# Kernel optimization log

Measured on AMD Instinct MI355X. Metric: run time of the kernel, lower is better.

Reference implementation:

```python
import jax, jax.numpy as jnp
import numpy as np

EPSILON = 0.05
MAX_ITER = 50
ALPHA = 6.0
THRESHOLD = 0.25
SCALE = 0.02  # keeps OT costs near THRESHOLD so the gate is not saturated


def setup_inputs() -> dict:
    key = jax.random.key(0)
    k1, k2 = jax.random.split(key)
    B, E, D, P = 8192, 8, 512, 32
    tokens = jax.random.normal(k1, (B, E, D), dtype=jnp.float32) * SCALE
    prototypes = jax.random.normal(k2, (E, P, D), dtype=jnp.float32) * SCALE
    return {"tokens": tokens, "prototypes": prototypes, "full_index": 0}


def _sinkhorn_log(cost, epsilon, max_iter):
    # cost: [..., n_source, n_target]; batched log-domain Sinkhorn, fixed iterations
    ns, nt = cost.shape[-2], cost.shape[-1]
    log_mu = jnp.full(cost.shape[:-1], -float(np.log(ns)), dtype=cost.dtype)
    log_nu = jnp.full(cost.shape[:-2] + (nt,), -float(np.log(nt)), dtype=cost.dtype)
    log_k = -cost / epsilon

    def step(carry, _):
        log_u, log_v = carry
        log_u = log_mu - jax.scipy.special.logsumexp(log_k + log_v[..., None, :], axis=-1)
        log_v = log_nu - jax.scipy.special.logsumexp(log_k + log_u[..., :, None], axis=-2)
        return (log_u, log_v), None

    (log_u, log_v), _ = jax.lax.scan(
        step, (jnp.zeros_like(log_mu), jnp.zeros_like(log_nu)), None, length=max_iter
    )
    return jnp.exp(log_k + log_u[..., :, None] + log_v[..., None, :])


def reference(tokens, prototypes, full_index):
    # tokens: [B, E, D], prototypes: [E, P, D]
    B, E, D = tokens.shape
    anchor = tokens[:, full_index, :]                                   # [B, D]
    source = jnp.stack(
        [tokens, jnp.broadcast_to(anchor[:, None, :], tokens.shape)], axis=2
    )                                                                   # [B, E, 2, D]
    # squared euclidean cdist: ||s||^2 - 2 s.p + ||p||^2
    s2 = jnp.sum(source * source, axis=-1)                              # [B, E, 2]
    p2 = jnp.sum(prototypes * prototypes, axis=-1)                      # [E, P]
    cross = jnp.einsum('besd,epd->besp', source, prototypes)            # [B, E, 2, P]
    cost = jnp.maximum(s2[..., None] - 2.0 * cross + p2[None, :, None, :], 0.0)
    transport = _sinkhorn_log(cost, EPSILON, MAX_ITER)                  # [B, E, 2, P]
    ot_cost = jnp.sum(transport * cost, axis=(-1, -2))                  # [B, E]
    validity = jax.nn.sigmoid(-ALPHA * (ot_cost - THRESHOLD))[..., None]  # [B, E, 1]
    # the full_index expert always passes with validity 1 and zero cost
    is_full = jnp.arange(E) == full_index                               # [E]
    ot_cost = jnp.where(is_full[None, :], 0.0, ot_cost)
    validity = jnp.where(is_full[None, :, None], 1.0, validity)
    return validity, ot_cost
```

## Files before the change

### kernel.cpp

```cpp
#include <hip/hip_runtime.h>
#include <hip/hip_bf16.h>


#define EXP2F(x) __builtin_amdgcn_exp2f(x)
#define LOG2F(x) __builtin_amdgcn_logf(x)
#define RCPF(x)  __builtin_amdgcn_rcpf(x)

typedef __bf16 bf16x8 __attribute__((ext_vector_type(8)));
typedef float  f32x4  __attribute__((ext_vector_type(4)));

#define BDIM 8192
#define EDIM 8
#define DDIM 512
#define PDIM 32
#define BPB  32
#define NTHR 256
#define PFD  4
#define C_SCALE 28.853900817779268f
#define LOG2E   1.4426950408889634f

__device__ __forceinline__ bf16x8 cvt2(float4 a, float4 b) {
  bf16x8 r;
  r[0] = (__bf16)a.x; r[1] = (__bf16)a.y; r[2] = (__bf16)a.z; r[3] = (__bf16)a.w;
  r[4] = (__bf16)b.x; r[5] = (__bf16)b.y; r[6] = (__bf16)b.z; r[7] = (__bf16)b.w;
  return r;
}

__global__ __launch_bounds__(NTHR, 3)
void ot_noise_gate_kernel(const float* __restrict__ tokens,
                          const float* __restrict__ protos,
                          const int*   __restrict__ fullIndexPtr,
                          float*       __restrict__ out) {
  const int fi    = fullIndexPtr[0];
  const int e     = blockIdx.x & (EDIM - 1);
  const int b0    = (blockIdx.x >> 3) * BPB;
  float* outVal = out;
  float* outOt  = out + BDIM * EDIM;

  if (e == fi) {
    int t = threadIdx.x;
    if (t < BPB) {
      int b = b0 + t;
      outVal[b * EDIM + e] = 1.0f;
      outOt [b * EDIM + e] = 0.0f;
    }
    return;
  }

  __shared__ __align__(16) __bf16 sB[64 * PDIM * 8];
  __shared__ float sPNp[8][PDIM];
  __shared__ __align__(16) float sCw[4][16][36];

  const int t  = threadIdx.x;
  const int l  = t & 63;
  const int w  = t >> 6;
  const int fr = l & 15;
  const int q4 = l >> 4;

  const int bRow = b0 + 8 * w + (fr & 7);
  const int eSel = (fr < 8) ? e : fi;
  const float4* rp4 = (const float4*)(tokens + ((size_t)bRow * EDIM + eSel) * DDIM);

  float4 buf[PFD][2];
  #pragma unroll
  for (int c = 0; c < PFD; ++c) {
    buf[c][0] = rp4[c * 8 + q4 * 2];
    buf[c][1] = rp4[c * 8 + q4 * 2 + 1];
  }

  {
    const float4* pG4 = (const float4*)(protos + (size_t)e * PDIM * DDIM);
    const int p  = t & 31;
    const int oh = t >> 5;
    float pnp = 0.f;
    #pragma unroll
    for (int pass = 0; pass < 8; ++pass) {
      int oct = oh * 8 + pass;
      float4 a = pG4[p * 128 + oct * 2];
      float4 b = pG4[p * 128 + oct * 2 + 1];
      pnp += a.x*a.x + a.y*a.y + a.z*a.z + a.w*a.w
           + b.x*b.x + b.y*b.y + b.z*b.z + b.w*b.w;
      *(bf16x8*)&sB[(oct * PDIM + p) * 8] = cvt2(a, b);
    }
    sPNp[oh][p] = pnp;
  }
  __syncthreads();

  f32x4 acc0 = (f32x4){0.f, 0.f, 0.f, 0.f};
  f32x4 acc1 = (f32x4){0.f, 0.f, 0.f, 0.f};
  float ss = 0.f;

  #pragma unroll
  for (int kc = 0; kc < 16; ++kc) {
    float4 ca0 = buf[kc % PFD][0];
    float4 ca1 = buf[kc % PFD][1];
    if (kc < 16 - PFD) {
      buf[kc % PFD][0] = rp4[(kc + PFD) * 8 + q4 * 2];
      buf[kc % PFD][1] = rp4[(kc + PFD) * 8 + q4 * 2 + 1];
    }
    ss += ca0.x*ca0.x + ca0.y*ca0.y + ca0.z*ca0.z + ca0.w*ca0.w
        + ca1.x*ca1.x + ca1.y*ca1.y + ca1.z*ca1.z + ca1.w*ca1.w;
    bf16x8 aF  = cvt2(ca0, ca1);
    bf16x8 bF0 = *(const bf16x8*)&sB[((kc * 4 + q4) * PDIM + fr) * 8];
    bf16x8 bF1 = *(const bf16x8*)&sB[((kc * 4 + q4) * PDIM + 16 + fr) * 8];
    acc0 = __builtin_amdgcn_mfma_f32_16x16x32_bf16(aF, bF0, acc0, 0, 0, 0);
    acc1 = __builtin_amdgcn_mfma_f32_16x16x32_bf16(aF, bF1, acc1, 0, 0, 0);
  }

  ss += __shfl_xor(ss, 16);
  ss += __shfl_xor(ss, 32);
  float pn_a = 0.f, pn_b = 0.f;
  #pragma unroll
  for (int o = 0; o < 8; ++o) {
    pn_a += sPNp[o][fr];
    pn_b += sPNp[o][16 + fr];
  }

  #pragma unroll
  for (int reg = 0; reg < 4; ++reg) {
    int row = q4 * 4 + reg;
    float nrm = __shfl(ss, row);
    sCw[w][row][fr]      = fmaxf(nrm - 2.f * acc0[reg] + pn_a, 0.f);
    sCw[w][row][16 + fr] = fmaxf(nrm - 2.f * acc1[reg] + pn_b, 0.f);
  }

  const int i = l & 7;
  const int s = l >> 3;
  float c0[4], c1[4];
  {
    float4 v0 = *(const float4*)&sCw[w][i][4 * s];
    float4 v1 = *(const float4*)&sCw[w][8 + i][4 * s];
    c0[0] = v0.x; c0[1] = v0.y; c0[2] = v0.z; c0[3] = v0.w;
    c1[0] = v1.x; c1[1] = v1.y; c1[2] = v1.z; c1[3] = v1.w;
  }

  float W[4], dc[4];
  float sum0 = 0.f, mA = -1e30f, mB = -1e30f;
  #pragma unroll
  for (int r = 0; r < 4; ++r) {
    float ka = -c0[r] * C_SCALE, kb = -c1[r] * C_SCALE;
    dc[r] = c1[r] - c0[r];
    sum0 += c0[r];
    mA = fmaxf(mA, ka);
    mB = fmaxf(mB, kb);
  }
  mA = fmaxf(mA, __shfl_xor(mA, 8));
  mA = fmaxf(mA, __shfl_xor(mA, 16));
  mA = fmaxf(mA, __shfl_xor(mA, 32));
  mB = fmaxf(mB, __shfl_xor(mB, 8));
  mB = fmaxf(mB, __shfl_xor(mB, 16));
  mB = fmaxf(mB, __shfl_xor(mB, 32));
  float sa = 0.f, sb = 0.f;
  #pragma unroll
  for (int r = 0; r < 4; ++r) {
    float ka = -c0[r] * C_SCALE, kb = -c1[r] * C_SCALE;
    sa += EXP2F(ka - mA);
    sb += EXP2F(kb - mB);
    W[r] = EXP2F(C_SCALE * dc[r]);
  }
  sa += __shfl_xor(sa, 8);  sa += __shfl_xor(sa, 16);  sa += __shfl_xor(sa, 32);
  sb += __shfl_xor(sb, 8);  sb += __shfl_xor(sb, 16);  sb += __shfl_xor(sb, 32);
  sum0 += __shfl_xor(sum0, 8);
  sum0 += __shfl_xor(sum0, 16);
  sum0 += __shfl_xor(sum0, 32);
  float delta = (mB + LOG2F(sb)) - (mA + LOG2F(sa));

  for (int it = 0; it < 49; ++it) {
    float s2 = EXP2F(delta);
    float T = 0.f;
    #pragma unroll
    for (int r = 0; r < 4; ++r)
      T += RCPF(__builtin_fmaf(W[r], s2, 1.0f));
    T += __shfl_xor(T, 8);
    T += __shfl_xor(T, 16);
    T += __shfl_xor(T, 32);
    float upd = LOG2F(T) - LOG2F(32.0f - T);
    delta += upd;
    if (__ballot(fabsf(upd) > 5e-7f) == 0ull) break;
  }

  float s2 = EXP2F(delta), sv = 0.f;
  #pragma unroll
  for (int r = 0; r < 4; ++r)
    sv += RCPF(__builtin_fmaf(W[r], s2, 1.0f)) * dc[r];
  sv += __shfl_xor(sv, 8);
  sv += __shfl_xor(sv, 16);
  sv += __shfl_xor(sv, 32);
  if (s == 0) {
    int b = b0 + 8 * w + i;
    float ot  = (sum0 + sv) * 0.03125f;
    float val = RCPF(1.0f + EXP2F(LOG2E * 6.0f * (ot - 0.25f)));
    outVal[b * EDIM + e] = val;
    outOt [b * EDIM + e] = ot;
  }
}

extern "C" void kernel_launch(void* const* d_in, const int* in_sizes, int n_in,
                              void* d_out, int out_size, void* d_ws, size_t ws_size,
                              hipStream_t stream) {
  const float* tokens = (const float*)d_in[0];
  const float* protos = (const float*)d_in[1];
  const int*   fidx   = (const int*)d_in[2];
  float* out = (float*)d_out;

  dim3 grid((BDIM / BPB) * EDIM);
  ot_noise_gate_kernel<<<grid, NTHR, 0, stream>>>(tokens, protos, fidx, out);
}
```

Before: 206.6 us.

## Use DPP row reductions and geometric extrapolation to end Sinkhorn iterations early

```diff
diff --git a/kernel.cpp b/kernel.cpp
--- a/kernel.cpp
+++ b/kernel.cpp
@@ -18,6 +18,24 @@
 #define PFD  4
 #define C_SCALE 28.853900817779268f
 #define LOG2E   1.4426950408889634f
+
+template<int CTRL>
+__device__ __forceinline__ float dpp_mov(float x) {
+  return __int_as_float(__builtin_amdgcn_update_dpp(
+      0, __float_as_int(x), CTRL, 0xF, 0xF, true));
+}
+__device__ __forceinline__ float dpp_sum8(float x) {
+  x += dpp_mov<0xB1>(x);
+  x += dpp_mov<0x4E>(x);
+  x += dpp_mov<0x141>(x);
+  return x;
+}
+__device__ __forceinline__ float dpp_max8(float x) {
+  x = fmaxf(x, dpp_mov<0xB1>(x));
+  x = fmaxf(x, dpp_mov<0x4E>(x));
+  x = fmaxf(x, dpp_mov<0x141>(x));
+  return x;
+}
 
 __device__ __forceinline__ bf16x8 cvt2(float4 a, float4 b) {
   bf16x8 r;
@@ -124,8 +142,8 @@
     sCw[w][row][16 + fr] = fmaxf(nrm - 2.f * acc1[reg] + pn_b, 0.f);
   }
 
-  const int i = l & 7;
-  const int s = l >> 3;
+  const int i = l >> 3;
+  const int s = l & 7;
   float c0[4], c1[4];
   {
     float4 v0 = *(const float4*)&sCw[w][i][4 * s];
@@ -144,12 +162,8 @@
     mA = fmaxf(mA, ka);
     mB = fmaxf(mB, kb);
   }
-  mA = fmaxf(mA, __shfl_xor(mA, 8));
-  mA = fmaxf(mA, __shfl_xor(mA, 16));
-  mA = fmaxf(mA, __shfl_xor(mA, 32));
-  mB = fmaxf(mB, __shfl_xor(mB, 8));
-  mB = fmaxf(mB, __shfl_xor(mB, 16));
-  mB = fmaxf(mB, __shfl_xor(mB, 32));
+  mA = dpp_max8(mA);
+  mB = dpp_max8(mB);
   float sa = 0.f, sb = 0.f;
   #pragma unroll
   for (int r = 0; r < 4; ++r) {
@@ -158,34 +172,42 @@
     sb += EXP2F(kb - mB);
     W[r] = EXP2F(C_SCALE * dc[r]);
   }
-  sa += __shfl_xor(sa, 8);  sa += __shfl_xor(sa, 16);  sa += __shfl_xor(sa, 32);
-  sb += __shfl_xor(sb, 8);  sb += __shfl_xor(sb, 16);  sb += __shfl_xor(sb, 32);
-  sum0 += __shfl_xor(sum0, 8);
-  sum0 += __shfl_xor(sum0, 16);
-  sum0 += __shfl_xor(sum0, 32);
+  sa   = dpp_sum8(sa);
+  sb   = dpp_sum8(sb);
+  sum0 = dpp_sum8(sum0);
   float delta = (mB + LOG2F(sb)) - (mA + LOG2F(sa));
 
+  float updPrev = delta;
+  float rPrev   = -1.f;
+  bool  live    = true;
   for (int it = 0; it < 49; ++it) {
     float s2 = EXP2F(delta);
     float T = 0.f;
     #pragma unroll
     for (int r = 0; r < 4; ++r)
       T += RCPF(__builtin_fmaf(W[r], s2, 1.0f));
-    T += __shfl_xor(T, 8);
-    T += __shfl_xor(T, 16);
-    T += __shfl_xor(T, 32);
+    T = dpp_sum8(T);
     float upd = LOG2F(T) - LOG2F(32.0f - T);
-    delta += upd;
-    if (__ballot(fabsf(upd) > 5e-7f) == 0ull) break;
+    float rr  = upd * RCPF(updPrev);
+    bool small = fabsf(upd) <= 5e-7f;
+    bool geo = live && !small && (it >= 3)
+             && (rr > 0.001f) && (rr < 0.998f)
+             && (fabsf(rr - rPrev) < 0.002f);
+    float mrem = (float)(48 - it);
+    float jump = geo
+        ? upd * rr * (1.0f - EXP2F(mrem * LOG2F(rr))) * RCPF(1.0f - rr)
+        : 0.0f;
+    if (live) delta += upd + jump;
+    live = live && !small && !geo;
+    rPrev = rr; updPrev = upd;
+    if (__ballot(live) == 0ull) break;
   }
 
   float s2 = EXP2F(delta), sv = 0.f;
   #pragma unroll
   for (int r = 0; r < 4; ++r)
     sv += RCPF(__builtin_fmaf(W[r], s2, 1.0f)) * dc[r];
-  sv += __shfl_xor(sv, 8);
-  sv += __shfl_xor(sv, 16);
-  sv += __shfl_xor(sv, 32);
+  sv = dpp_sum8(sv);
   if (s == 0) {
     int b = b0 + 8 * w + i;
     float ot  = (sum0 + sv) * 0.03125f;
```

Result: no change. 206.0 us (-0.3%).
